# Optimization experiments

Hardware: AMD Instinct MI355X
Metric: run time of the kernel (lower is better)

## Reference

```python
import jax, jax.numpy as jnp
import numpy as np

B, S, H = 128, 512, 256
STEP = 1


def setup_inputs() -> dict:
    key = jax.random.key(0)
    ks = jax.random.split(key, 16)
    stdv = 1.0 / np.sqrt(H)
    u = lambda k, shape: jax.random.uniform(k, shape, jnp.float32, -stdv, stdv)
    return {
        "A": jax.random.uniform(ks[0], (B, S, 2 * S), jnp.float32),
        "hidden": jax.random.normal(ks[1], (B, S, H), jnp.float32),
        "mask": jnp.ones((B, S), jnp.int32),
        # linear_edge_in / linear_edge_out (Linear(H, H, bias=True))
        "W_in": u(ks[2], (H, H)),  "b_in": u(ks[3], (H,)),
        "W_out": u(ks[4], (H, H)), "b_out": u(ks[5], (H,)),
        # adjacency biases
        "b_iah": u(ks[6], (H,)), "b_oah": u(ks[7], (H,)),
        # GRU-style gate weights: w_ih [3H, 2H], w_hh [3H, H]
        "w_ih": u(ks[8], (3 * H, 2 * H)), "b_ih": u(ks[9], (3 * H,)),
        "w_hh": u(ks[10], (3 * H, H)),    "b_hh": u(ks[11], (3 * H,)),
    }


def _gnn_cell(A, hidden, W_in, b_in, W_out, b_out, b_iah, b_oah,
              w_ih, b_ih, w_hh, b_hh):
    s = hidden.shape[1]
    # edge-transformed features (torch F.linear: x @ W.T + b)
    h_in = jnp.einsum('bsh,gh->bsg', hidden, W_in) + b_in
    h_out = jnp.einsum('bsh,gh->bsg', hidden, W_out) + b_out
    # adjacency message passing: [B,S,S] @ [B,S,H]
    input_in = jnp.einsum('bij,bjh->bih', A[:, :, :s], h_in) + b_iah
    input_out = jnp.einsum('bij,bjh->bih', A[:, :, s:2 * s], h_out) + b_oah
    inputs = jnp.concatenate([input_in, input_out], axis=2)  # [B,S,2H]
    gi = jnp.einsum('bsi,gi->bsg', inputs, w_ih) + b_ih      # [B,S,3H]
    gh = jnp.einsum('bsh,gh->bsg', hidden, w_hh) + b_hh      # [B,S,3H]
    i_r, i_i, i_n = jnp.split(gi, 3, axis=2)
    h_r, h_i, h_n = jnp.split(gh, 3, axis=2)
    resetgate = jax.nn.sigmoid(i_r + h_r)
    inputgate = jax.nn.sigmoid(i_i + h_i)
    newgate = jnp.tanh(i_n + resetgate * h_n)
    return hidden + inputgate * (newgate - hidden)


def reference(A, hidden, mask, W_in, b_in, W_out, b_out, b_iah, b_oah,
              w_ih, b_ih, w_hh, b_hh):
    # GNN.forward with issrgnn=True: run GNNCell `step` times (mask unused)
    for _ in range(STEP):
        hidden = _gnn_cell(A, hidden, W_in, b_in, W_out, b_out,
                           b_iah, b_oah, w_ih, b_ih, w_hh, b_hh)
    return hidden
```

## Files before the change

kernel.cpp:

```cpp
#include <hip/hip_runtime.h>

#define B_ 128
#define S_ 512
#define H_ 256
#define M_ (B_*S_)

typedef __attribute__((ext_vector_type(4))) float f32x4;
typedef __attribute__((ext_vector_type(8))) short s16x8;
typedef __attribute__((ext_vector_type(4))) unsigned short u16x4;
typedef unsigned short ushort_t;

typedef __attribute__((address_space(1))) void as1_void;
typedef __attribute__((address_space(3))) void as3_void;

__device__ __forceinline__ unsigned short f2h(float f) {
  _Float16 h = (_Float16)f;
  return __builtin_bit_cast(unsigned short, h);
}
__device__ __forceinline__ float h2f(ushort_t u) {
  return (float)__builtin_bit_cast(_Float16, u);
}

__device__ __forceinline__ f32x4 mfma16(s16x8 a, s16x8 b, f32x4 c) {
  asm("v_mfma_f32_16x16x32_f16 %0, %1, %2, %0" : "+v"(c) : "v"(a), "v"(b));
  return c;
}

__device__ __forceinline__ void cp16(const void* g, void* l) {
  __builtin_amdgcn_global_load_lds((as1_void*)g, (as3_void*)l, 16, 0, 0);
}

__device__ __forceinline__ void waitvm(int n) {
  switch (n) {
    case 0:  asm volatile("s_waitcnt vmcnt(0)"  ::: "memory"); break;
    case 4:  asm volatile("s_waitcnt vmcnt(4)"  ::: "memory"); break;
    case 5:  asm volatile("s_waitcnt vmcnt(5)"  ::: "memory"); break;
    case 6:  asm volatile("s_waitcnt vmcnt(6)"  ::: "memory"); break;
    case 8:  asm volatile("s_waitcnt vmcnt(8)"  ::: "memory"); break;
    case 12: asm volatile("s_waitcnt vmcnt(12)" ::: "memory"); break;
  }
}

__device__ __forceinline__ int stage_kc(int lane) {
  return (lane & 3) ^ ((lane >> 3) & 3);
}
__device__ __forceinline__ int frag_off(int s, int lane) {
  int ln = lane & 15, kg = lane >> 4;
  return s * 512 + (ln * 4 + (kg ^ ((ln >> 1) & 3))) * 8;
}

__global__ void k_cvt_all(const float* __restrict__ hidden, ushort_t* __restrict__ hidh,
                          const float* __restrict__ W_in,  const float* __restrict__ W_out,
                          ushort_t* __restrict__ wcat,
                          const float* __restrict__ w_ih, ushort_t* __restrict__ wihh,
                          const float* __restrict__ w_hh, ushort_t* __restrict__ whhh) {
  int blk = blockIdx.x;
  const float* src; ushort_t* dst; int base;
  if (blk < 8192)      { src = hidden; dst = hidh;           base = blk; }
  else if (blk < 8224) { src = W_in;   dst = wcat;           base = blk - 8192; }
  else if (blk < 8256) { src = W_out;  dst = wcat + 65536;   base = blk - 8224; }
  else if (blk < 8448) { src = w_ih;   dst = wihh;           base = blk - 8256; }
  else                 { src = w_hh;   dst = whhh;           base = blk - 8448; }
  int i = base * 256 + threadIdx.x;
  const float* p = src + (size_t)i * 8;
  f32x4 a = *(const f32x4*)p;
  f32x4 b = *(const f32x4*)(p + 4);
  s16x8 o;
  o[0]=(short)f2h(a[0]); o[1]=(short)f2h(a[1]); o[2]=(short)f2h(a[2]); o[3]=(short)f2h(a[3]);
  o[4]=(short)f2h(b[0]); o[5]=(short)f2h(b[1]); o[6]=(short)f2h(b[2]); o[7]=(short)f2h(b[3]);
  *(s16x8*)(dst + (size_t)i * 8) = o;
}

__global__ __launch_bounds__(256, 2)
void k_gemm1(const ushort_t* __restrict__ hid, const ushort_t* __restrict__ wcat,
             const float* __restrict__ b_in, const float* __restrict__ b_out,
             ushort_t* __restrict__ hcatT) {
  __shared__ __attribute__((aligned(16))) ushort_t lA[3][8*512];
  __shared__ __attribute__((aligned(16))) ushort_t lB[3][16*512];
  const int flat = blockIdx.y * 8 + blockIdx.x;
  const int orig = (flat & 7) * 128 + (flat >> 3);
  const int bx = orig & 7, bb = orig >> 3;
  const int j0 = (bx >> 1) * 128;
  const int n0 = (bx & 1) * 256;
  const int tid = threadIdx.x;
  const int w = tid >> 6, lane = tid & 63;
  const int ln = lane & 15, kg = lane >> 4;
  const int wm = w >> 1, wn = w & 1;
  const int srow = lane >> 2, skc = stage_kc(lane);

  f32x4 acc[4][8];
  #pragma unroll
  for (int i = 0; i < 4; ++i)
    #pragma unroll
    for (int j = 0; j < 8; ++j) acc[i][j] = (f32x4){0.f,0.f,0.f,0.f};

  const size_t arow0 = (size_t)bb * 512 + j0;

  auto stage = [&](int t, int bsel) {
    int k0 = t * 32;
    #pragma unroll
    for (int it = 0; it < 2; ++it) {
      int s = it*4 + w;
      cp16(hid + (arow0 + s*16 + srow)*256 + k0 + skc*8, &lA[bsel][s*512]);
    }
    #pragma unroll
    for (int it = 0; it < 4; ++it) {
      int s = it*4 + w;
      cp16(wcat + (size_t)(n0 + s*16 + srow)*256 + k0 + skc*8, &lB[bsel][s*512]);
    }
  };
  auto compute = [&](int cur) {
    s16x8 af[4];
    #pragma unroll
    for (int mf = 0; mf < 4; ++mf)
      af[mf] = *(const s16x8*)&lA[cur][frag_off(wm*4 + mf, lane)];
    __builtin_amdgcn_s_setprio(1);
    #pragma unroll
    for (int nf = 0; nf < 8; ++nf) {
      s16x8 bf = *(const s16x8*)&lB[cur][frag_off(wn*8 + nf, lane)];
      #pragma unroll
      for (int mf = 0; mf < 4; ++mf) acc[mf][nf] = mfma16(af[mf], bf, acc[mf][nf]);
    }
    __builtin_amdgcn_s_setprio(0);
  };

  stage(0, 0); stage(1, 1);
  for (int t = 0; t < 6; ++t) {
    waitvm(6);
    __builtin_amdgcn_s_barrier();
    stage(t + 2, (t + 2) % 3);
    compute(t % 3);
  }
  waitvm(6); __builtin_amdgcn_s_barrier(); compute(6 % 3);
  waitvm(0); __builtin_amdgcn_s_barrier(); compute(7 % 3);

  #pragma unroll
  for (int nf = 0; nf < 8; ++nf) {
    int gn = n0 + wn*128 + nf*16 + ln;
    float bias = (gn < 256) ? b_in[gn] : b_out[gn - 256];
    #pragma unroll
    for (int mf = 0; mf < 4; ++mf) {
      int j = j0 + wm*64 + mf*16 + kg*4;
      u16x4 v;
      #pragma unroll
      for (int r = 0; r < 4; ++r) v[r] = f2h(acc[mf][nf][r] + bias);
      *(u16x4*)&hcatT[((size_t)(bb*512 + gn))*512 + j] = v;
    }
  }
}

__global__ __launch_bounds__(256, 2)
void k_gemm2(const float* __restrict__ A, const ushort_t* __restrict__ hcatT,
             const float* __restrict__ b_iah, const float* __restrict__ b_oah,
             ushort_t* __restrict__ inp) {
  __shared__ __attribute__((aligned(16))) ushort_t lA[2][8*512];
  __shared__ __attribute__((aligned(16))) ushort_t lB[3][16*512];
  const int flat = blockIdx.y * 8 + blockIdx.x;
  const int orig = (flat & 7) * 128 + (flat >> 3);
  const int bx = orig & 7, bb = orig >> 3;
  const int i0 = (bx >> 1) * 128;
  const int half = bx & 1;
  const int n0 = half * 256;
  const int tid = threadIdx.x;
  const int w = tid >> 6, lane = tid & 63;
  const int ln = lane & 15, kg = lane >> 4;
  const int wm = w >> 1, wn = w & 1;
  const int srow = lane >> 2, skc = stage_kc(lane);

  f32x4 acc[4][8];
  #pragma unroll
  for (int i = 0; i < 4; ++i)
    #pragma unroll
    for (int j = 0; j < 8; ++j) acc[i][j] = (f32x4){0.f,0.f,0.f,0.f};

  const float* Abase = A + ((size_t)bb*512 + i0)*1024 + half*512;
  f32x4 ra[2][4];

  auto loadA = [&](int t, f32x4 (&r)[4]) {
    int k0 = t * 32;
    #pragma unroll
    for (int it = 0; it < 2; ++it) {
      int s = it*4 + w;
      const float* p = Abase + (size_t)(s*16 + srow)*1024 + k0 + skc*8;
      r[it*2]   = *(const f32x4*)p;
      r[it*2+1] = *(const f32x4*)(p + 4);
    }
  };
  auto stageB = [&](int t, int bsel) {
    int k0 = t * 32;
    #pragma unroll
    for (int it = 0; it < 4; ++it) {
      int s = it*4 + w;
      cp16(hcatT + ((size_t)(bb*512 + n0 + s*16 + srow))*512 + k0 + skc*8, &lB[bsel][s*512]);
    }
  };
  auto writeA = [&](const f32x4 (&r)[4], int bsel) {
    #pragma unroll
    for (int it = 0; it < 2; ++it) {
      int s = it*4 + w;
      s16x8 o;
      o[0]=(short)f2h(r[it*2][0]); o[1]=(short)f2h(r[it*2][1]);
      o[2]=(short)f2h(r[it*2][2]); o[3]=(short)f2h(r[it*2][3]);
      o[4]=(short)f2h(r[it*2+1][0]); o[5]=(short)f2h(r[it*2+1][1]);
      o[6]=(short)f2h(r[it*2+1][2]); o[7]=(short)f2h(r[it*2+1][3]);
      *(s16x8*)&lA[bsel][s*512 + lane*8] = o;
    }
  };
  auto compute = [&](int acur, int bcur) {
    s16x8 af[4];
    #pragma unroll
    for (int mf = 0; mf < 4; ++mf)
      af[mf] = *(const s16x8*)&lA[acur][frag_off(wm*4 + mf, lane)];
    __builtin_amdgcn_s_setprio(1);
    #pragma unroll
    for (int nf = 0; nf < 8; ++nf) {
      s16x8 bf = *(const s16x8*)&lB[bcur][frag_off(wn*8 + nf, lane)];
      #pragma unroll
      for (int mf = 0; mf < 4; ++mf) acc[mf][nf] = mfma16(af[mf], bf, acc[mf][nf]);
    }
    __builtin_amdgcn_s_setprio(0);
  };

  loadA(0, ra[0]); stageB(0, 0);
  loadA(1, ra[1]); stageB(1, 1);
  waitvm(12);
  writeA(ra[0], 0);
  asm volatile("s_waitcnt lgkmcnt(0)" ::: "memory");

  #pragma unroll
  for (int t = 0; t < 16; ++t) {
    waitvm(t < 15 ? 8 : 0);
    __builtin_amdgcn_s_barrier();
    if (t + 2 < 16) { loadA(t + 2, ra[t & 1]); stageB(t + 2, (t + 2) % 3); }
    compute(t & 1, t % 3);
    if (t + 1 < 16) {
      waitvm(t + 2 < 16 ? 12 : 4);
      writeA(ra[(t + 1) & 1], (t + 1) & 1);
      asm volatile("s_waitcnt lgkmcnt(0)" ::: "memory");
    }
  }

  #pragma unroll
  for (int nf = 0; nf < 8; ++nf) {
    int gn = n0 + wn*128 + nf*16 + ln;
    float bias = half ? b_oah[gn - 256] : b_iah[gn];
    #pragma unroll
    for (int mf = 0; mf < 4; ++mf) {
      #pragma unroll
      for (int r = 0; r < 4; ++r) {
        int i = i0 + wm*64 + mf*16 + kg*4 + r;
        inp[((size_t)(bb*512 + i))*512 + gn] = f2h(acc[mf][nf][r] + bias);
      }
    }
  }
}

__global__ __launch_bounds__(256, 2)
void k_gemm3(const ushort_t* __restrict__ inp, const ushort_t* __restrict__ hidh,
             const ushort_t* __restrict__ wih, const ushort_t* __restrict__ whh,
             const float* __restrict__ b_ih, const float* __restrict__ b_hh,
             float* __restrict__ out) {
  __shared__ __attribute__((aligned(16))) ushort_t lIn[3][8*512];
  __shared__ __attribute__((aligned(16))) ushort_t lW[3][12*512];
  const int flat = blockIdx.y * 4 + blockIdx.x;
  const int orig = (flat & 7) * 256 + (flat >> 3);
  const int h0 = (orig & 3) * 64;
  const int m0 = (orig >> 2) * 128;
  const int tid = threadIdx.x;
  const int w = tid >> 6, lane = tid & 63;
  const int ln = lane & 15, kg = lane >> 4;
  const int wm2 = w >> 1, wh = w & 1;
  const int srow = lane >> 2, skc = stage_kc(lane);

  f32x4 aR[4][2], aI[4][2], aIN[4][2], aHN[4][2];
  #pragma unroll
  for (int m = 0; m < 4; ++m)
    #pragma unroll
    for (int n = 0; n < 2; ++n) {
      aR[m][n] = (f32x4){0.f,0.f,0.f,0.f}; aI[m][n] = (f32x4){0.f,0.f,0.f,0.f};
      aIN[m][n] = (f32x4){0.f,0.f,0.f,0.f}; aHN[m][n] = (f32x4){0.f,0.f,0.f,0.f};
    }

  auto stage = [&](int gs, int bsel) {
    if (gs < 16) {
      int k0 = gs * 32;
      #pragma unroll
      for (int it = 0; it < 2; ++it) {
        int s = it*4 + w;
        cp16(inp + (size_t)(m0 + s*16 + srow)*512 + k0 + skc*8, &lIn[bsel][s*512]);
      }
      #pragma unroll
      for (int it = 0; it < 3; ++it) {
        int s = it*4 + w;
        int row = s*16 + srow, g = row >> 6, r = row & 63;
        cp16(wih + (size_t)(g*256 + h0 + r)*512 + k0 + skc*8, &lW[bsel][s*512]);
      }
    } else {
      int k0 = (gs - 16) * 32;
      #pragma unroll
      for (int it = 0; it < 2; ++it) {
        int s = it*4 + w;
        cp16(hidh + (size_t)(m0 + s*16 + srow)*256 + k0 + skc*8, &lIn[bsel][s*512]);
      }
      #pragma unroll
      for (int it = 0; it < 3; ++it) {
        int s = it*4 + w;
        int row = s*16 + srow, g = row >> 6, r = row & 63;
        cp16(whh + (size_t)(g*256 + h0 + r)*256 + k0 + skc*8, &lW[bsel][s*512]);
      }
    }
  };

  auto compute = [&](int cur, f32x4 (&aN)[4][2]) {
    s16x8 af[4];
    #pragma unroll
    for (int mf = 0; mf < 4; ++mf)
      af[mf] = *(const s16x8*)&lIn[cur][frag_off(wm2*4 + mf, lane)];
    __builtin_amdgcn_s_setprio(1);
    #pragma unroll
    for (int g = 0; g < 3; ++g) {
      #pragma unroll
      for (int nf = 0; nf < 2; ++nf) {
        s16x8 bf = *(const s16x8*)&lW[cur][frag_off(g*4 + wh*2 + nf, lane)];
        #pragma unroll
        for (int mf = 0; mf < 4; ++mf) {
          f32x4& a = (g == 0 ? aR[mf][nf] : g == 1 ? aI[mf][nf] : aN[mf][nf]);
          a = mfma16(af[mf], bf, a);
        }
      }
    }
    __builtin_amdgcn_s_setprio(0);
  };

  stage(0, 0);
  stage(1, 1);
  for (int t = 0; t < 16; ++t) {
    waitvm(5);
    __builtin_amdgcn_s_barrier();
    stage(t + 2, (t + 2) % 3);
    compute(t % 3, aIN);
  }
  for (int t = 16; t < 22; ++t) {
    waitvm(5);
    __builtin_amdgcn_s_barrier();
    stage(t + 2, (t + 2) % 3);
    compute(t % 3, aHN);
  }
  waitvm(5); __builtin_amdgcn_s_barrier(); compute(22 % 3, aHN);
  waitvm(0); __builtin_amdgcn_s_barrier(); compute(23 % 3, aHN);

  #pragma unroll
  for (int nf = 0; nf < 2; ++nf) {
    int h = h0 + wh*32 + nf*16 + ln;
    float br  = b_ih[h]       + b_hh[h];
    float bi  = b_ih[256 + h] + b_hh[256 + h];
    float bni = b_ih[512 + h];
    float bnh = b_hh[512 + h];
    #pragma unroll
    for (int mf = 0; mf < 4; ++mf) {
      #pragma unroll
      for (int r = 0; r < 4; ++r) {
        int m = m0 + wm2*64 + mf*16 + kg*4 + r;
        float rg = 1.0f / (1.0f + __expf(-(aR[mf][nf][r] + br)));
        float ig = 1.0f / (1.0f + __expf(-(aI[mf][nf][r] + bi)));
        float narg = aIN[mf][nf][r] + bni + rg * (aHN[mf][nf][r] + bnh);
        float e2 = __expf(2.0f * narg);
        float ng = 1.0f - 2.0f / (e2 + 1.0f);
        float hv = h2f(hidh[(size_t)m*256 + h]);
        out[(size_t)m*256 + h] = hv + ig * (ng - hv);
      }
    }
  }
}

extern "C" void kernel_launch(void* const* d_in, const int* in_sizes, int n_in,
                              void* d_out, int out_size, void* d_ws, size_t ws_size,
                              hipStream_t stream) {
  const float* A      = (const float*)d_in[0];
  const float* hidden = (const float*)d_in[1];
  const float* W_in   = (const float*)d_in[3];
  const float* b_in   = (const float*)d_in[4];
  const float* W_out  = (const float*)d_in[5];
  const float* b_out  = (const float*)d_in[6];
  const float* b_iah  = (const float*)d_in[7];
  const float* b_oah  = (const float*)d_in[8];
  const float* w_ih   = (const float*)d_in[9];
  const float* b_ih   = (const float*)d_in[10];
  const float* w_hh   = (const float*)d_in[11];
  const float* b_hh   = (const float*)d_in[12];
  float* out = (float*)d_out;

  char* ws = (char*)d_ws;
  ushort_t* hidh  = (ushort_t*)(ws);
  ushort_t* wcat  = (ushort_t*)(ws + 33554432);
  ushort_t* wihh  = (ushort_t*)(ws + 33816576);
  ushort_t* whhh  = (ushort_t*)(ws + 34603008);
  ushort_t* hcatT = (ushort_t*)(ws + 34996224);
  ushort_t* inp   = (ushort_t*)(ws + 102105088);

  k_cvt_all<<<8544, 256, 0, stream>>>(hidden, hidh, W_in, W_out, wcat,
                                      w_ih, wihh, w_hh, whhh);

  k_gemm1<<<dim3(8, 128), 256, 0, stream>>>(hidh, wcat, b_in, b_out, hcatT);
  k_gemm2<<<dim3(8, 128), 256, 0, stream>>>(A, hcatT, b_iah, b_oah, inp);
  k_gemm3<<<dim3(4, 512), 256, 0, stream>>>(inp, hidh, wihh, whhh, b_ih, b_hh, out);
}
```

Baseline: 264.2 us.

## Fuse hidden fp32-to-fp16 conversion into first GEMM's A-tile load

```diff
diff --git a/kernel.cpp b/kernel.cpp
--- a/kernel.cpp
+++ b/kernel.cpp
@@ -49,18 +49,16 @@
   return s * 512 + (ln * 4 + (kg ^ ((ln >> 1) & 3))) * 8;
 }
 
-__global__ void k_cvt_all(const float* __restrict__ hidden, ushort_t* __restrict__ hidh,
-                          const float* __restrict__ W_in,  const float* __restrict__ W_out,
-                          ushort_t* __restrict__ wcat,
-                          const float* __restrict__ w_ih, ushort_t* __restrict__ wihh,
-                          const float* __restrict__ w_hh, ushort_t* __restrict__ whhh) {
+__global__ void k_cvt_w(const float* __restrict__ W_in,  const float* __restrict__ W_out,
+                        ushort_t* __restrict__ wcat,
+                        const float* __restrict__ w_ih, ushort_t* __restrict__ wihh,
+                        const float* __restrict__ w_hh, ushort_t* __restrict__ whhh) {
   int blk = blockIdx.x;
   const float* src; ushort_t* dst; int base;
-  if (blk < 8192)      { src = hidden; dst = hidh;           base = blk; }
-  else if (blk < 8224) { src = W_in;   dst = wcat;           base = blk - 8192; }
-  else if (blk < 8256) { src = W_out;  dst = wcat + 65536;   base = blk - 8224; }
-  else if (blk < 8448) { src = w_ih;   dst = wihh;           base = blk - 8256; }
-  else                 { src = w_hh;   dst = whhh;           base = blk - 8448; }
+  if (blk < 32)       { src = W_in;  dst = wcat;         base = blk; }
+  else if (blk < 64)  { src = W_out; dst = wcat + 65536; base = blk - 32; }
+  else if (blk < 256) { src = w_ih;  dst = wihh;         base = blk - 64; }
+  else                { src = w_hh;  dst = whhh;         base = blk - 256; }
   int i = base * 256 + threadIdx.x;
   const float* p = src + (size_t)i * 8;
   f32x4 a = *(const f32x4*)p;
@@ -72,10 +70,10 @@
 }
 
 __global__ __launch_bounds__(256, 2)
-void k_gemm1(const ushort_t* __restrict__ hid, const ushort_t* __restrict__ wcat,
+void k_gemm1(const float* __restrict__ hid, const ushort_t* __restrict__ wcat,
              const float* __restrict__ b_in, const float* __restrict__ b_out,
-             ushort_t* __restrict__ hcatT) {
-  __shared__ __attribute__((aligned(16))) ushort_t lA[3][8*512];
+             ushort_t* __restrict__ hcatT, ushort_t* __restrict__ hidh) {
+  __shared__ __attribute__((aligned(16))) ushort_t lA[2][8*512];
   __shared__ __attribute__((aligned(16))) ushort_t lB[3][16*512];
   const int flat = blockIdx.y * 8 + blockIdx.x;
   const int orig = (flat & 7) * 128 + (flat >> 3);
@@ -94,45 +92,72 @@
     #pragma unroll
     for (int j = 0; j < 8; ++j) acc[i][j] = (f32x4){0.f,0.f,0.f,0.f};
 
-  const size_t arow0 = (size_t)bb * 512 + j0;
-
-  auto stage = [&](int t, int bsel) {
+  const float* Abase = hid + ((size_t)bb*512 + j0)*256;
+  f32x4 ra[2][4];
+
+  auto loadA = [&](int t, f32x4 (&r)[4]) {
     int k0 = t * 32;
     #pragma unroll
     for (int it = 0; it < 2; ++it) {
       int s = it*4 + w;
-      cp16(hid + (arow0 + s*16 + srow)*256 + k0 + skc*8, &lA[bsel][s*512]);
-    }
+      const float* p = Abase + (size_t)(s*16 + srow)*256 + k0 + skc*8;
+      r[it*2]   = *(const f32x4*)p;
+      r[it*2+1] = *(const f32x4*)(p + 4);
+    }
+  };
+  auto stageB = [&](int t, int bsel) {
+    int k0 = t * 32;
     #pragma unroll
     for (int it = 0; it < 4; ++it) {
       int s = it*4 + w;
       cp16(wcat + (size_t)(n0 + s*16 + srow)*256 + k0 + skc*8, &lB[bsel][s*512]);
     }
   };
-  auto compute = [&](int cur) {
+  auto writeA = [&](const f32x4 (&r)[4], int bsel) {
+    #pragma unroll
+    for (int it = 0; it < 2; ++it) {
+      int s = it*4 + w;
+      s16x8 o;
+      o[0]=(short)f2h(r[it*2][0]); o[1]=(short)f2h(r[it*2][1]);
+      o[2]=(short)f2h(r[it*2][2]); o[3]=(short)f2h(r[it*2][3]);
+      o[4]=(short)f2h(r[it*2+1][0]); o[5]=(short)f2h(r[it*2+1][1]);
+      o[6]=(short)f2h(r[it*2+1][2]); o[7]=(short)f2h(r[it*2+1][3]);
+      *(s16x8*)&lA[bsel][s*512 + lane*8] = o;
+    }
+  };
+  auto compute = [&](int acur, int bcur) {
     s16x8 af[4];
     #pragma unroll
     for (int mf = 0; mf < 4; ++mf)
-      af[mf] = *(const s16x8*)&lA[cur][frag_off(wm*4 + mf, lane)];
+      af[mf] = *(const s16x8*)&lA[acur][frag_off(wm*4 + mf, lane)];
     __builtin_amdgcn_s_setprio(1);
     #pragma unroll
     for (int nf = 0; nf < 8; ++nf) {
-      s16x8 bf = *(const s16x8*)&lB[cur][frag_off(wn*8 + nf, lane)];
+      s16x8 bf = *(const s16x8*)&lB[bcur][frag_off(wn*8 + nf, lane)];
       #pragma unroll
       for (int mf = 0; mf < 4; ++mf) acc[mf][nf] = mfma16(af[mf], bf, acc[mf][nf]);
     }
     __builtin_amdgcn_s_setprio(0);
   };
 
-  stage(0, 0); stage(1, 1);
-  for (int t = 0; t < 6; ++t) {
-    waitvm(6);
+  loadA(0, ra[0]); stageB(0, 0);
+  loadA(1, ra[1]); stageB(1, 1);
+  waitvm(12);
+  writeA(ra[0], 0);
+  asm volatile("s_waitcnt lgkmcnt(0)" ::: "memory");
+
+  #pragma unroll
+  for (int t = 0; t < 8; ++t) {
+    waitvm(t < 7 ? 8 : 0);
     __builtin_amdgcn_s_barrier();
-    stage(t + 2, (t + 2) % 3);
-    compute(t % 3);
-  }
-  waitvm(6); __builtin_amdgcn_s_barrier(); compute(6 % 3);
-  waitvm(0); __builtin_amdgcn_s_barrier(); compute(7 % 3);
+    if (t + 2 < 8) { loadA(t + 2, ra[t & 1]); stageB(t + 2, (t + 2) % 3); }
+    compute(t & 1, t % 3);
+    if (t + 1 < 8) {
+      waitvm(t + 2 < 8 ? 12 : 4);
+      writeA(ra[(t + 1) & 1], (t + 1) & 1);
+      asm volatile("s_waitcnt lgkmcnt(0)" ::: "memory");
+    }
+  }
 
   #pragma unroll
   for (int nf = 0; nf < 8; ++nf) {
@@ -145,6 +170,20 @@
       #pragma unroll
       for (int r = 0; r < 4; ++r) v[r] = f2h(acc[mf][nf][r] + bias);
       *(u16x4*)&hcatT[((size_t)(bb*512 + gn))*512 + j] = v;
+    }
+  }
+
+  if (n0 == 0) {
+    const size_t base = ((size_t)bb*512 + j0) * 256;
+    #pragma unroll
+    for (int i = 0; i < 16; ++i) {
+      size_t e = base + ((size_t)i*256 + tid) * 8;
+      f32x4 a = *(const f32x4*)(hid + e);
+      f32x4 b = *(const f32x4*)(hid + e + 4);
+      s16x8 o;
+      o[0]=(short)f2h(a[0]); o[1]=(short)f2h(a[1]); o[2]=(short)f2h(a[2]); o[3]=(short)f2h(a[3]);
+      o[4]=(short)f2h(b[0]); o[5]=(short)f2h(b[1]); o[6]=(short)f2h(b[2]); o[7]=(short)f2h(b[3]);
+      *(s16x8*)(hidh + e) = o;
     }
   }
 }
@@ -398,10 +437,9 @@
   ushort_t* hcatT = (ushort_t*)(ws + 34996224);
   ushort_t* inp   = (ushort_t*)(ws + 102105088);
 
-  k_cvt_all<<<8544, 256, 0, stream>>>(hidden, hidh, W_in, W_out, wcat,
-                                      w_ih, wihh, w_hh, whhh);
-
-  k_gemm1<<<dim3(8, 128), 256, 0, stream>>>(hidh, wcat, b_in, b_out, hcatT);
+  k_cvt_w<<<352, 256, 0, stream>>>(W_in, W_out, wcat, w_ih, wihh, w_hh, whhh);
+
+  k_gemm1<<<dim3(8, 128), 256, 0, stream>>>(hidden, wcat, b_in, b_out, hcatT, hidh);
   k_gemm2<<<dim3(8, 128), 256, 0, stream>>>(A, hcatT, b_iah, b_oah, inp);
   k_gemm3<<<dim3(4, 512), 256, 0, stream>>>(inp, hidh, wihh, whhh, b_ih, b_hh, out);
 }
```

New measurement: 270.5 us. +2.4%, slower.
